# Kernel tuning notes

Hardware: AMD Instinct MI355X
Metric: run time of the kernel (lower is better)

## Reference

```python
import jax, jax.numpy as jnp
import numpy as np

B, IN, E, NCLS = 1024, 784, 256, 10
BRAIN, ADIM, NJUMPS = 4, 3, 4
N = BRAIN ** ADIM  # 64 blocks
TAU = 1.0
_GKEY = jax.random.key(42)  # fixed key -> deterministic gumbel noise


def _gumbel_softmax_hard(key, logits):
    u = jax.random.uniform(key, logits.shape, minval=1e-6, maxval=1.0 - 1e-6)
    g = -jnp.log(-jnp.log(u))
    y = jax.nn.softmax((logits + g) / TAU, axis=-1)
    hard = jax.nn.one_hot(jnp.argmax(y, axis=-1), logits.shape[-1], dtype=y.dtype)
    return jax.lax.stop_gradient(hard - y) + y  # straight-through


def _next_address(state, key, at0_W1, at0_b1, at0_W2, at0_b2):
    # always uses block 0's address_transform (as in the original forward)
    h = jax.nn.relu(state @ at0_W1 + at0_b1)
    logits = (h @ at0_W2 + at0_b2).reshape(state.shape[0], ADIM, BRAIN)
    return _gumbel_softmax_hard(key, logits)  # (B, ADIM, BRAIN) one-hot


def _all_blocks(state, st_W1, st_b1, st_W2, st_b2):
    # state: (B,E); st_W*: (N,E,E) stored (in,out). Two batched GEMMs over all N blocks.
    h = jax.nn.relu(jnp.einsum('be,neh->bnh', state, st_W1) + st_b1[None])
    h = jax.nn.relu(jnp.einsum('bnh,nhg->bng', h, st_W2) + st_b2[None])
    norm = jnp.linalg.norm(state, axis=1, keepdims=True)  # (B,1), norm of INPUT state
    return h / (norm[:, :, None] + 1e-6)  # (B,N,E)


def _flatten_onehot(oh):
    # (B, ADIM, BRAIN) -> (B, BRAIN**ADIM) via iterated outer product
    b = oh.shape[0]
    fw = oh[:, 0, :]
    for d in range(1, oh.shape[1]):
        fw = (fw[:, :, None] * oh[:, d, None, :]).reshape(b, -1)
    return fw


def _forward(x, W_emb, b_emb, st_W1, st_b1, st_W2, st_b2,
             at0_W1, at0_b1, at0_W2, at0_b2, out_W1, out_b1, out_W2, out_b2):
    bsz = x.shape[0]
    state = x.reshape(bsz, -1) @ W_emb + b_emb
    initial_state = state
    current_address = _next_address(state, jax.random.fold_in(_GKEY, 0),
                                    at0_W1, at0_b1, at0_W2, at0_b2)
    exited = jnp.zeros((bsz,), dtype=bool)
    exit_states = jnp.zeros_like(state)
    exit_addresses = jnp.zeros_like(current_address)
    for i in range(NJUMPS):  # fixed small jump count; early-break replaced by masking (same math)
        active = ~exited
        bw = _flatten_onehot(current_address)                      # (B,N)
        allout = _all_blocks(state, st_W1, st_b1, st_W2, st_b2)    # (B,N,E)
        new_state = jnp.einsum('bn,bne->be', bw, allout)
        new_address = _next_address(new_state, jax.random.fold_in(_GKEY, i + 1),
                                    at0_W1, at0_b1, at0_W2, at0_b2)
        idx = jnp.argmax(new_address, axis=2)
        is_origin = jnp.all(idx == 0, axis=1) & active
        exit_states = jnp.where(is_origin[:, None], new_state, exit_states)
        exit_addresses = jnp.where(is_origin[:, None, None], new_address, exit_addresses)
        exited = exited | is_origin
        state = jnp.where(active[:, None], new_state, state)
        current_address = jnp.where(active[:, None, None], new_address, current_address)
    final_address = jnp.where(exited[:, None, None], exit_addresses, current_address)
    bw = _flatten_onehot(final_address)
    # original code computes block_out twice and keeps the one using `state` (bug-faithful)
    allout = _all_blocks(state, st_W1, st_b1, st_W2, st_b2)
    final_output = jnp.einsum('bn,bne->be', bw, allout) + initial_state
    h = jax.nn.relu(final_output @ out_W1 + out_b1)
    return h @ out_W2 + out_b2  # (B, NCLS)


def setup_inputs() -> dict:
    key = jax.random.key(0)
    ks = jax.random.split(key, 16)
    s = 0.02
    return {
        'x': jax.random.normal(ks[0], (B, IN), jnp.float32),
        'W_emb': jax.random.normal(ks[1], (IN, E), jnp.float32) * s,
        'b_emb': jnp.zeros((E,), jnp.float32),
        'st_W1': jax.random.normal(ks[2], (N, E, E), jnp.float32) * s,
        'st_b1': jnp.zeros((N, E), jnp.float32),
        'st_W2': jax.random.normal(ks[3], (N, E, E), jnp.float32) * s,
        'st_b2': jnp.zeros((N, E), jnp.float32),
        'at0_W1': jax.random.normal(ks[4], (E, E), jnp.float32) * s,
        'at0_b1': jnp.zeros((E,), jnp.float32),
        'at0_W2': jax.random.normal(ks[5], (E, ADIM * BRAIN), jnp.float32) * s,
        'at0_b2': jnp.zeros((ADIM * BRAIN,), jnp.float32),
        'out_W1': jax.random.normal(ks[6], (E, E), jnp.float32) * s,
        'out_b1': jnp.zeros((E,), jnp.float32),
        'out_W2': jax.random.normal(ks[7], (E, NCLS), jnp.float32) * s,
        'out_b2': jnp.zeros((NCLS,), jnp.float32),
    }


def reference(x, W_emb, b_emb, st_W1, st_b1, st_W2, st_b2,
              at0_W1, at0_b1, at0_W2, at0_b2, out_W1, out_b1, out_W2, out_b2):
    return _forward(x, W_emb, b_emb, st_W1, st_b1, st_W2, st_b2,
                    at0_W1, at0_b1, at0_W2, at0_b2, out_W1, out_b1, out_W2, out_b2)
```

## Files before the change

kernel.cpp:

```cpp
#include <hip/hip_runtime.h>
#include <stdint.h>


#define BATCH 1024
#define EDIM  256
#define INDIM 784
#define GRID_BE 192

__host__ __device__ inline uint32_t rotl32(uint32_t x, uint32_t d) {
  return (x << d) | (x >> (32u - d));
}
__host__ __device__ inline void threefry2x32(uint32_t k0, uint32_t k1,
                                             uint32_t x0, uint32_t x1,
                                             uint32_t* o0, uint32_t* o1) {
  uint32_t ks2 = k0 ^ k1 ^ 0x1BD11BDAu;
  x0 += k0; x1 += k1;
#define TF_R(a) { x0 += x1; x1 = rotl32(x1, a); x1 ^= x0; }
  TF_R(13) TF_R(15) TF_R(26) TF_R(6)   x0 += k1;  x1 += ks2 + 1u;
  TF_R(17) TF_R(29) TF_R(16) TF_R(24)  x0 += ks2; x1 += k0  + 2u;
  TF_R(13) TF_R(15) TF_R(26) TF_R(6)   x0 += k0;  x1 += k1  + 3u;
  TF_R(17) TF_R(29) TF_R(16) TF_R(24)  x0 += k1;  x1 += ks2 + 4u;
  TF_R(13) TF_R(15) TF_R(26) TF_R(6)   x0 += ks2; x1 += k0  + 5u;
#undef TF_R
  *o0 = x0; *o1 = x1;
}
__device__ inline uint32_t jax_bits12288(uint32_t k0, uint32_t k1, uint32_t L) {
  uint32_t o0, o1;
  if (L < 6144u) { threefry2x32(k0, k1, L, L + 6144u, &o0, &o1); return o0; }
  else           { threefry2x32(k0, k1, L - 6144u, L, &o0, &o1); return o1; }
}
__device__ inline float jax_uniform(uint32_t bits) {
  const float minv = 1e-6f;
  const float maxv = (float)(1.0 - 1e-06);
  const float span = maxv - minv;
  uint32_t fb = (bits >> 9) | 0x3f800000u;
  float f = __uint_as_float(fb) - 1.0f;
  float u = __fadd_rn(__fmul_rn(f, span), minv);
  return fmaxf(minv, u);
}

__global__ __launch_bounds__(1024) void k_embed(
    const float* __restrict__ x, const float* __restrict__ Wemb,
    const float* __restrict__ bemb,
    float* __restrict__ stateA, float* __restrict__ initial,
    int* __restrict__ count0) {
  __shared__ float XS[8 * INDIM];
  __shared__ float P[8][128][9];
  const int t = threadIdx.x;
  if (blockIdx.x == 0 && t < 64) count0[t] = 0;
  const int rg = blockIdx.x >> 1, ch = blockIdx.x & 1;
  const int jl = t & 127, ks = t >> 7;

  {
    const float4* src = (const float4*)(x + (size_t)rg * 8 * INDIM);
    float4* dst = (float4*)XS;
    for (int p = t; p < (8 * INDIM) / 4; p += 1024) dst[p] = src[p];
  }
  __syncthreads();

  const int col = ch * 128 + jl;
  const int kb = (ks < 4) ? ks * 100 : 400 + (ks - 4) * 96;
  const int ke = kb + ((ks < 4) ? 100 : 96);
  float a[8] = {0.f,0.f,0.f,0.f,0.f,0.f,0.f,0.f};
#pragma unroll 2
  for (int k = kb; k < ke; k += 4) {
    const float w0 = Wemb[(k+0)*EDIM + col], w1 = Wemb[(k+1)*EDIM + col],
                w2 = Wemb[(k+2)*EDIM + col], w3 = Wemb[(k+3)*EDIM + col];
#pragma unroll
    for (int i = 0; i < 8; i++) {
      const float4 s4 = *(const float4*)&XS[i * INDIM + k];
      a[i] = fmaf(s4.x, w0, a[i]); a[i] = fmaf(s4.y, w1, a[i]);
      a[i] = fmaf(s4.z, w2, a[i]); a[i] = fmaf(s4.w, w3, a[i]);
    }
  }
#pragma unroll
  for (int q = 0; q < 8; q++) P[ks][jl][q] = a[q];
  __syncthreads();
  {
    const int c2 = t & 127, i = t >> 7;
    float s = 0.f;
#pragma unroll
    for (int w = 0; w < 8; w++) s += P[w][c2][i];
    s += bemb[ch * 128 + c2];
    const size_t idx = (size_t)(rg * 8 + i) * EDIM + ch * 128 + c2;
    stateA[idx] = s; initial[idx] = s;
  }
}

__global__ __launch_bounds__(1024) void k_addr(
    const float* __restrict__ state,
    const float* __restrict__ aW1, const float* __restrict__ ab1,
    const float* __restrict__ aW2, const float* __restrict__ ab2,
    int* __restrict__ exited, int* __restrict__ n_next, int* __restrict__ count,
    float* __restrict__ sout, int step, uint32_t fk0, uint32_t fk1) {
  __shared__ float XS[4 * EDIM];
  __shared__ float P[4][256][5];
  __shared__ float H[EDIM][4];
  __shared__ float P2[16][4][16];
  __shared__ float vals[4][12];
  __shared__ int   flags[4];
  const int t = threadIdx.x, b0 = blockIdx.x * 4;

  XS[t] = state[(size_t)b0 * EDIM + t];
  __syncthreads();

  const int j = t & 255, ks = t >> 8;
  const int kb = ks * 64;
  float a[4] = {0.f,0.f,0.f,0.f};
#pragma unroll 2
  for (int k = kb; k < kb + 64; k += 4) {
    const float w0 = aW1[(k+0)*EDIM + j], w1 = aW1[(k+1)*EDIM + j],
                w2 = aW1[(k+2)*EDIM + j], w3 = aW1[(k+3)*EDIM + j];
#pragma unroll
    for (int i = 0; i < 4; i++) {
      const float4 s4 = *(const float4*)&XS[i * EDIM + k];
      a[i] = fmaf(s4.x, w0, a[i]); a[i] = fmaf(s4.y, w1, a[i]);
      a[i] = fmaf(s4.z, w2, a[i]); a[i] = fmaf(s4.w, w3, a[i]);
    }
  }
#pragma unroll
  for (int q = 0; q < 4; q++) P[ks][j][q] = a[q];
  __syncthreads();
  {
    const int j2 = t & 255, i = t >> 8;
    float s = P[0][j2][i] + P[1][j2][i] + P[2][j2][i] + P[3][j2][i] + ab1[j2];
    H[j2][i] = fmaxf(s, 0.f);
  }
  __syncthreads();
  {
    const int c = t & 15, i = (t >> 4) & 3, ksl = t >> 6;
    float a2 = 0.f;
    if (c < 12) {
      const int k0 = ksl * 16;
#pragma unroll 4
      for (int k = k0; k < k0 + 16; k++)
        a2 = fmaf(H[k][i], aW2[k * 12 + c], a2);
    }
    P2[ksl][i][c] = a2;
  }
  __syncthreads();
  if (t < 48) {
    const int i = t / 12, c = t % 12;
    float s = 0.f;
#pragma unroll
    for (int w = 0; w < 16; w++) s += P2[w][i][c];
    const float logit = s + ab2[c];
    const uint32_t L = (uint32_t)((b0 + i) * 12 + c);
    const float u = jax_uniform(jax_bits12288(fk0, fk1, L));
    const float g = -logf(-logf(u));
    vals[i][c] = logit + g;
  }
  __syncthreads();
  if (t < 4) {
    const int b = b0 + t;
    int idx0 = 0, idx1 = 0, idx2 = 0;
    { float best = vals[t][0];
#pragma unroll
      for (int c = 1; c < 4; c++) { float v = vals[t][c];     if (v > best) { best = v; idx0 = c; } } }
    { float best = vals[t][4];
#pragma unroll
      for (int c = 1; c < 4; c++) { float v = vals[t][4 + c]; if (v > best) { best = v; idx1 = c; } } }
    { float best = vals[t][8];
#pragma unroll
      for (int c = 1; c < 4; c++) { float v = vals[t][8 + c]; if (v > best) { best = v; idx2 = c; } } }
    const int nn = idx0 * 16 + idx1 * 4 + idx2;
    int nxt;
    if (step == 0)      { exited[b] = 0; nxt = nn; }
    else if (step < 4)  {
      if (exited[b])      nxt = -1;
      else if (nn == 0) { exited[b] = 1; nxt = -1; }
      else                nxt = nn;
    } else                nxt = exited[b] ? 0 : nn;
    n_next[b] = nxt; flags[t] = nxt;
    if (nxt >= 0) atomicAdd(&count[nxt], 1);
  }
  __syncthreads();
  {
    const int i = t >> 8, jj = t & 255;
    if (flags[i] < 0) sout[(size_t)(b0 + i) * EDIM + jj] = XS[i * EDIM + jj];
  }
}

__global__ __launch_bounds__(1024) void k_blocks(
    const float* __restrict__ sin,
    const float* __restrict__ W1, const float* __restrict__ b1,
    const float* __restrict__ W2, const float* __restrict__ b2,
    const int* __restrict__ count, const int* __restrict__ n_next,
    const float* __restrict__ initial, float* __restrict__ sout,
    int* __restrict__ count_next, int is_final) {
  __shared__ float XS[8 * EDIM];
  __shared__ float P[4][256][9];
  __shared__ float H[EDIM][12];
  __shared__ int   meta[4];
  __shared__ int   rowsl[8];
  __shared__ float denom[8];
  __shared__ int   wcnt[16], wbase[16];
  const int t = threadIdx.x, c = blockIdx.x;
  if (c == 0 && t < 64) count_next[t] = 0;
  if (t < 8) rowsl[t] = 0;
  if (t < 64) {
    const int cnt = count[t];
    const int nch = (cnt + 7) >> 3;
    int icnt = cnt, inch = nch;
#pragma unroll
    for (int d = 1; d < 64; d <<= 1) {
      int t1 = __shfl_up(icnt, d), t2 = __shfl_up(inch, d);
      if (t >= d) { icnt += t1; inch += t2; }
    }
    const int ench = inch - nch;
    const int total = __shfl(inch, 63);
    if (t == 0) meta[3] = total;
    if (c >= ench && c < ench + nch) {
      meta[0] = t; meta[1] = c - ench;
      meta[2] = min(8, cnt - (c - ench) * 8);
    }
  }
  __syncthreads();
  if (c >= meta[3]) return;
  const int n = meta[0], local = meta[1], m = meta[2];

  {
    const bool flag = (n_next[t] == n);
    const unsigned long long bal = __ballot(flag);
    const int wid = t >> 6, lane = t & 63;
    if (lane == 0) wcnt[wid] = __popcll(bal);
    __syncthreads();
    if (t == 0) { int s = 0; for (int w = 0; w < 16; w++) { wbase[w] = s; s += wcnt[w]; } }
    __syncthreads();
    if (flag) {
      const int rank = wbase[wid] + __popcll(bal & ((1ull << lane) - 1ull));
      const int r0 = local * 8;
      if (rank >= r0 && rank < r0 + 8) rowsl[rank - r0] = t;
    }
    __syncthreads();
  }

  if (t < 512) {
    const int i = t >> 6, q = t & 63;
    const int row = rowsl[min(i, m - 1)] & 1023;
    const float4 v = *(const float4*)(sin + (size_t)row * EDIM + q * 4);
    ((float4*)XS)[t] = v;
    float sq = v.x*v.x + v.y*v.y + v.z*v.z + v.w*v.w;
#pragma unroll
    for (int d = 32; d >= 1; d >>= 1) sq += __shfl_xor(sq, d);
    if (q == 0) denom[i] = sqrtf(sq) + 1e-6f;
  }
  __syncthreads();

  const int j = t & 255, ks = t >> 8;
  const int kb = ks * 64;
  const float* W1n = W1 + (size_t)n * EDIM * EDIM;
  {
    float a[8] = {0.f,0.f,0.f,0.f,0.f,0.f,0.f,0.f};
#pragma unroll 2
    for (int k = kb; k < kb + 64; k += 4) {
      const float w0 = W1n[(k+0)*EDIM + j], w1 = W1n[(k+1)*EDIM + j],
                  w2 = W1n[(k+2)*EDIM + j], w3 = W1n[(k+3)*EDIM + j];
#pragma unroll
      for (int i = 0; i < 8; i++) {
        const float4 s4 = *(const float4*)&XS[i * EDIM + k];
        a[i] = fmaf(s4.x, w0, a[i]); a[i] = fmaf(s4.y, w1, a[i]);
        a[i] = fmaf(s4.z, w2, a[i]); a[i] = fmaf(s4.w, w3, a[i]);
      }
    }
#pragma unroll
    for (int q = 0; q < 8; q++) P[ks][j][q] = a[q];
  }
  __syncthreads();
  {
    const int j2 = t & 255, ih = t >> 8;
    const float bb = b1[(size_t)n * EDIM + j2];
#pragma unroll
    for (int qq = 0; qq < 2; qq++) {
      const int i = ih + qq * 4;
      float s = P[0][j2][i] + P[1][j2][i] + P[2][j2][i] + P[3][j2][i] + bb;
      H[j2][i] = fmaxf(s, 0.f);
    }
  }
  __syncthreads();
  const float* W2n = W2 + (size_t)n * EDIM * EDIM;
  {
    float a[8] = {0.f,0.f,0.f,0.f,0.f,0.f,0.f,0.f};
#pragma unroll 4
    for (int k = kb; k < kb + 64; k++) {
      const float w = W2n[k*EDIM + j];
      const float4 h0 = *(const float4*)&H[k][0];
      const float4 h1 = *(const float4*)&H[k][4];
      a[0] = fmaf(h0.x, w, a[0]); a[1] = fmaf(h0.y, w, a[1]);
      a[2] = fmaf(h0.z, w, a[2]); a[3] = fmaf(h0.w, w, a[3]);
      a[4] = fmaf(h1.x, w, a[4]); a[5] = fmaf(h1.y, w, a[5]);
      a[6] = fmaf(h1.z, w, a[6]); a[7] = fmaf(h1.w, w, a[7]);
    }
#pragma unroll
    for (int q = 0; q < 8; q++) P[ks][j][q] = a[q];
  }
  __syncthreads();
  {
    const int col = t & 255, ih = t >> 8;
    const float bb2 = b2[(size_t)n * EDIM + col];
#pragma unroll
    for (int qq = 0; qq < 2; qq++) {
      const int i = ih + qq * 4;
      if (i < m) {
        float s = P[0][col][i] + P[1][col][i] + P[2][col][i] + P[3][col][i] + bb2;
        float v = fmaxf(s, 0.f) / denom[i];
        const int row = rowsl[i] & 1023;
        if (is_final) v += initial[(size_t)row * EDIM + col];
        sout[(size_t)row * EDIM + col] = v;
      }
    }
  }
}

__global__ __launch_bounds__(1024) void k_head(
    const float* __restrict__ fin,
    const float* __restrict__ oW1, const float* __restrict__ ob1,
    const float* __restrict__ oW2, const float* __restrict__ ob2,
    float* __restrict__ out) {
  __shared__ float XS[4 * EDIM];
  __shared__ float P[4][256][5];
  __shared__ float H[EDIM][4];
  __shared__ float P2[16][4][16];
  const int t = threadIdx.x, b0 = blockIdx.x * 4;
  XS[t] = fin[(size_t)b0 * EDIM + t];
  __syncthreads();
  const int j = t & 255, ks = t >> 8;
  const int kb = ks * 64;
  float a[4] = {0.f,0.f,0.f,0.f};
#pragma unroll 2
  for (int k = kb; k < kb + 64; k += 4) {
    const float w0 = oW1[(k+0)*EDIM + j], w1 = oW1[(k+1)*EDIM + j],
                w2 = oW1[(k+2)*EDIM + j], w3 = oW1[(k+3)*EDIM + j];
#pragma unroll
    for (int i = 0; i < 4; i++) {
      const float4 s4 = *(const float4*)&XS[i * EDIM + k];
      a[i] = fmaf(s4.x, w0, a[i]); a[i] = fmaf(s4.y, w1, a[i]);
      a[i] = fmaf(s4.z, w2, a[i]); a[i] = fmaf(s4.w, w3, a[i]);
    }
  }
#pragma unroll
  for (int q = 0; q < 4; q++) P[ks][j][q] = a[q];
  __syncthreads();
  {
    const int j2 = t & 255, i = t >> 8;
    float s = P[0][j2][i] + P[1][j2][i] + P[2][j2][i] + P[3][j2][i] + ob1[j2];
    H[j2][i] = fmaxf(s, 0.f);
  }
  __syncthreads();
  {
    const int c = t & 15, i = (t >> 4) & 3, ksl = t >> 6;
    float a2 = 0.f;
    if (c < 10) {
      const int k0 = ksl * 16;
#pragma unroll 4
      for (int k = k0; k < k0 + 16; k++)
        a2 = fmaf(H[k][i], oW2[k * 10 + c], a2);
    }
    P2[ksl][i][c] = a2;
  }
  __syncthreads();
  if (t < 40) {
    const int i = t / 10, c = t % 10;
    float s = 0.f;
#pragma unroll
    for (int w = 0; w < 16; w++) s += P2[w][i][c];
    out[(size_t)(b0 + i) * 10 + c] = s + ob2[c];
  }
}

extern "C" void kernel_launch(void* const* d_in, const int* in_sizes, int n_in,
                              void* d_out, int out_size, void* d_ws, size_t ws_size,
                              hipStream_t stream) {
  const float* x    = (const float*)d_in[0];
  const float* Wemb = (const float*)d_in[1];
  const float* bemb = (const float*)d_in[2];
  const float* stW1 = (const float*)d_in[3];
  const float* stb1 = (const float*)d_in[4];
  const float* stW2 = (const float*)d_in[5];
  const float* stb2 = (const float*)d_in[6];
  const float* aW1  = (const float*)d_in[7];
  const float* ab1  = (const float*)d_in[8];
  const float* aW2  = (const float*)d_in[9];
  const float* ab2  = (const float*)d_in[10];
  const float* oW1  = (const float*)d_in[11];
  const float* ob1  = (const float*)d_in[12];
  const float* oW2  = (const float*)d_in[13];
  const float* ob2  = (const float*)d_in[14];
  float* out = (float*)d_out;

  char* ws = (char*)d_ws;
  auto alloc = [&](size_t bytes) { char* p = ws; ws += (bytes + 255) & ~(size_t)255; return p; };
  float* stateA  = (float*)alloc((size_t)BATCH * EDIM * 4);
  float* stateB  = (float*)alloc((size_t)BATCH * EDIM * 4);
  float* initial = (float*)alloc((size_t)BATCH * EDIM * 4);
  float* finalb  = (float*)alloc((size_t)BATCH * EDIM * 4);
  int* exited = (int*)alloc(BATCH * 4);
  int* n_next = (int*)alloc(BATCH * 4);
  int* counters[2];
  counters[0] = (int*)alloc(64 * 4);
  counters[1] = (int*)alloc(64 * 4);

  uint32_t fk0[5], fk1[5];
  for (uint32_t s = 0; s < 5; s++) threefry2x32(0u, 42u, 0u, s, &fk0[s], &fk1[s]);

  k_embed<<<256, 1024, 0, stream>>>(x, Wemb, bemb, stateA, initial, counters[0]);

  float* cur = stateA;
  float* nxt = stateB;
  for (int j = 0; j < 5; j++) {
    int* cnt  = counters[j & 1];
    int* cntN = counters[(j + 1) & 1];
    float* dst = (j < 4) ? nxt : finalb;
    k_addr<<<BATCH / 4, 1024, 0, stream>>>(cur, aW1, ab1, aW2, ab2,
        exited, n_next, cnt, dst, j, fk0[j], fk1[j]);
    k_blocks<<<GRID_BE, 1024, 0, stream>>>(cur, stW1, stb1, stW2, stb2,
        cnt, n_next, initial, dst, cntN, (j == 4) ? 1 : 0);
    if (j < 4) { float* tmp = cur; cur = nxt; nxt = tmp; }
  }
  k_head<<<BATCH / 4, 1024, 0, stream>>>(finalb, oW1, ob1, oW2, ob2, out);
}
```

Before: 265.9 us.

## Fuse address routing into block kernels and head into final block kernel

Merges the embedding and first address computation into one kernel, fuses each jump's address MLP and gumbel argmax into the block-expert kernel, and folds the output head into the final block kernel. Per-block routing counts are rebuilt locally from a per-step routing array, which drops the global atomic counters, the exited array and the ping-pong state buffers. Launches go from twelve to six and the state round-trips between them are removed. In exchange, each block recomputes a histogram over the whole batch, and the address MLP runs on padded groups of eight rows.

```diff
diff --git a/kernel.cpp b/kernel.cpp
--- a/kernel.cpp
+++ b/kernel.cpp
@@ -5,7 +5,7 @@
 #define BATCH 1024
 #define EDIM  256
 #define INDIM 784
-#define GRID_BE 192
+#define GRID_B 192
 
 __host__ __device__ inline uint32_t rotl32(uint32_t x, uint32_t d) {
   return (x << d) | (x >> (32u - d));
@@ -38,97 +38,98 @@
   float u = __fadd_rn(__fmul_rn(f, span), minv);
   return fmaxf(minv, u);
 }
-
-__global__ __launch_bounds__(1024) void k_embed(
+__device__ inline float gumbel_val(int s, int b, int c) {
+  uint32_t fk0, fk1;
+  threefry2x32(0u, 42u, 0u, (uint32_t)s, &fk0, &fk1);
+  const uint32_t L = (uint32_t)(b * 12 + c);
+  const float u = jax_uniform(jax_bits12288(fk0, fk1, L));
+  return -logf(-logf(u));
+}
+
+__device__ inline int addr_argmax(const float* v) {
+  int i0 = 0, i1 = 0, i2 = 0;
+  { float b = v[0];
+    for (int c = 1; c < 4; c++) { float x = v[c];     if (x > b) { b = x; i0 = c; } } }
+  { float b = v[4];
+    for (int c = 1; c < 4; c++) { float x = v[4 + c]; if (x > b) { b = x; i1 = c; } } }
+  { float b = v[8];
+    for (int c = 1; c < 4; c++) { float x = v[8 + c]; if (x > b) { b = x; i2 = c; } } }
+  return i0 * 16 + i1 * 4 + i2;
+}
+
+__global__ __launch_bounds__(1024, 4) void k_embed_a0(
     const float* __restrict__ x, const float* __restrict__ Wemb,
     const float* __restrict__ bemb,
-    float* __restrict__ stateA, float* __restrict__ initial,
-    int* __restrict__ count0) {
-  __shared__ float XS[8 * INDIM];
-  __shared__ float P[8][128][9];
-  const int t = threadIdx.x;
-  if (blockIdx.x == 0 && t < 64) count0[t] = 0;
-  const int rg = blockIdx.x >> 1, ch = blockIdx.x & 1;
-  const int jl = t & 127, ks = t >> 7;
-
-  {
-    const float4* src = (const float4*)(x + (size_t)rg * 8 * INDIM);
-    float4* dst = (float4*)XS;
-    for (int p = t; p < (8 * INDIM) / 4; p += 1024) dst[p] = src[p];
-  }
-  __syncthreads();
-
-  const int col = ch * 128 + jl;
-  const int kb = (ks < 4) ? ks * 100 : 400 + (ks - 4) * 96;
-  const int ke = kb + ((ks < 4) ? 100 : 96);
-  float a[8] = {0.f,0.f,0.f,0.f,0.f,0.f,0.f,0.f};
-#pragma unroll 2
-  for (int k = kb; k < ke; k += 4) {
-    const float w0 = Wemb[(k+0)*EDIM + col], w1 = Wemb[(k+1)*EDIM + col],
-                w2 = Wemb[(k+2)*EDIM + col], w3 = Wemb[(k+3)*EDIM + col];
-#pragma unroll
-    for (int i = 0; i < 8; i++) {
-      const float4 s4 = *(const float4*)&XS[i * INDIM + k];
-      a[i] = fmaf(s4.x, w0, a[i]); a[i] = fmaf(s4.y, w1, a[i]);
-      a[i] = fmaf(s4.z, w2, a[i]); a[i] = fmaf(s4.w, w3, a[i]);
-    }
-  }
-#pragma unroll
-  for (int q = 0; q < 8; q++) P[ks][jl][q] = a[q];
-  __syncthreads();
-  {
-    const int c2 = t & 127, i = t >> 7;
-    float s = 0.f;
-#pragma unroll
-    for (int w = 0; w < 8; w++) s += P[w][c2][i];
-    s += bemb[ch * 128 + c2];
-    const size_t idx = (size_t)(rg * 8 + i) * EDIM + ch * 128 + c2;
-    stateA[idx] = s; initial[idx] = s;
-  }
-}
-
-__global__ __launch_bounds__(1024) void k_addr(
-    const float* __restrict__ state,
     const float* __restrict__ aW1, const float* __restrict__ ab1,
     const float* __restrict__ aW2, const float* __restrict__ ab2,
-    int* __restrict__ exited, int* __restrict__ n_next, int* __restrict__ count,
-    float* __restrict__ sout, int step, uint32_t fk0, uint32_t fk1) {
-  __shared__ float XS[4 * EDIM];
+    float* __restrict__ state, float* __restrict__ initial,
+    int* __restrict__ nn_all) {
+  __shared__ float XS[4 * INDIM];
   __shared__ float P[4][256][5];
+  __shared__ float SS[4 * EDIM];
   __shared__ float H[EDIM][4];
   __shared__ float P2[16][4][16];
   __shared__ float vals[4][12];
-  __shared__ int   flags[4];
   const int t = threadIdx.x, b0 = blockIdx.x * 4;
 
-  XS[t] = state[(size_t)b0 * EDIM + t];
+  {
+    const float4* src = (const float4*)(x + (size_t)b0 * INDIM);
+    float4* dst = (float4*)XS;
+    for (int p = t; p < INDIM; p += 1024) dst[p] = src[p];
+  }
   __syncthreads();
 
   const int j = t & 255, ks = t >> 8;
-  const int kb = ks * 64;
-  float a[4] = {0.f,0.f,0.f,0.f};
+  {
+    const int kb = ks * 196;
+    float a[4] = {0.f,0.f,0.f,0.f};
 #pragma unroll 2
-  for (int k = kb; k < kb + 64; k += 4) {
-    const float w0 = aW1[(k+0)*EDIM + j], w1 = aW1[(k+1)*EDIM + j],
-                w2 = aW1[(k+2)*EDIM + j], w3 = aW1[(k+3)*EDIM + j];
-#pragma unroll
-    for (int i = 0; i < 4; i++) {
-      const float4 s4 = *(const float4*)&XS[i * EDIM + k];
-      a[i] = fmaf(s4.x, w0, a[i]); a[i] = fmaf(s4.y, w1, a[i]);
-      a[i] = fmaf(s4.z, w2, a[i]); a[i] = fmaf(s4.w, w3, a[i]);
-    }
-  }
-#pragma unroll
-  for (int q = 0; q < 4; q++) P[ks][j][q] = a[q];
+    for (int k = kb; k < kb + 196; k += 4) {
+      const float w0 = Wemb[(k+0)*EDIM + j], w1 = Wemb[(k+1)*EDIM + j],
+                  w2 = Wemb[(k+2)*EDIM + j], w3 = Wemb[(k+3)*EDIM + j];
+#pragma unroll
+      for (int i = 0; i < 4; i++) {
+        const float4 s4 = *(const float4*)&XS[i * INDIM + k];
+        a[i] = fmaf(s4.x, w0, a[i]); a[i] = fmaf(s4.y, w1, a[i]);
+        a[i] = fmaf(s4.z, w2, a[i]); a[i] = fmaf(s4.w, w3, a[i]);
+      }
+    }
+#pragma unroll
+    for (int q = 0; q < 4; q++) P[ks][j][q] = a[q];
+  }
   __syncthreads();
   {
     const int j2 = t & 255, i = t >> 8;
+    float s = P[0][j2][i] + P[1][j2][i] + P[2][j2][i] + P[3][j2][i] + bemb[j2];
+    SS[i * EDIM + j2] = s;
+    const size_t idx = (size_t)(b0 + i) * EDIM + j2;
+    state[idx] = s; initial[idx] = s;
+  }
+  __syncthreads();
+
+  { const int kb = ks * 64;
+    float a[4] = {0.f,0.f,0.f,0.f};
+#pragma unroll 2
+    for (int k = kb; k < kb + 64; k += 4) {
+      const float w0 = aW1[(k+0)*EDIM + j], w1 = aW1[(k+1)*EDIM + j],
+                  w2 = aW1[(k+2)*EDIM + j], w3 = aW1[(k+3)*EDIM + j];
+#pragma unroll
+      for (int i = 0; i < 4; i++) {
+        const float4 s4 = *(const float4*)&SS[i * EDIM + k];
+        a[i] = fmaf(s4.x, w0, a[i]); a[i] = fmaf(s4.y, w1, a[i]);
+        a[i] = fmaf(s4.z, w2, a[i]); a[i] = fmaf(s4.w, w3, a[i]);
+      }
+    }
+#pragma unroll
+    for (int q = 0; q < 4; q++) P[ks][j][q] = a[q];
+  }
+  __syncthreads();
+  { const int j2 = t & 255, i = t >> 8;
     float s = P[0][j2][i] + P[1][j2][i] + P[2][j2][i] + P[3][j2][i] + ab1[j2];
     H[j2][i] = fmaxf(s, 0.f);
   }
   __syncthreads();
-  {
-    const int c = t & 15, i = (t >> 4) & 3, ksl = t >> 6;
+  { const int c = t & 15, i = (t >> 4) & 3, ksl = t >> 6;
     float a2 = 0.f;
     if (c < 12) {
       const int k0 = ksl * 16;
@@ -144,62 +145,44 @@
     float s = 0.f;
 #pragma unroll
     for (int w = 0; w < 16; w++) s += P2[w][i][c];
-    const float logit = s + ab2[c];
-    const uint32_t L = (uint32_t)((b0 + i) * 12 + c);
-    const float u = jax_uniform(jax_bits12288(fk0, fk1, L));
-    const float g = -logf(-logf(u));
-    vals[i][c] = logit + g;
-  }
-  __syncthreads();
-  if (t < 4) {
-    const int b = b0 + t;
-    int idx0 = 0, idx1 = 0, idx2 = 0;
-    { float best = vals[t][0];
-#pragma unroll
-      for (int c = 1; c < 4; c++) { float v = vals[t][c];     if (v > best) { best = v; idx0 = c; } } }
-    { float best = vals[t][4];
-#pragma unroll
-      for (int c = 1; c < 4; c++) { float v = vals[t][4 + c]; if (v > best) { best = v; idx1 = c; } } }
-    { float best = vals[t][8];
-#pragma unroll
-      for (int c = 1; c < 4; c++) { float v = vals[t][8 + c]; if (v > best) { best = v; idx2 = c; } } }
-    const int nn = idx0 * 16 + idx1 * 4 + idx2;
-    int nxt;
-    if (step == 0)      { exited[b] = 0; nxt = nn; }
-    else if (step < 4)  {
-      if (exited[b])      nxt = -1;
-      else if (nn == 0) { exited[b] = 1; nxt = -1; }
-      else                nxt = nn;
-    } else                nxt = exited[b] ? 0 : nn;
-    n_next[b] = nxt; flags[t] = nxt;
-    if (nxt >= 0) atomicAdd(&count[nxt], 1);
-  }
-  __syncthreads();
-  {
-    const int i = t >> 8, jj = t & 255;
-    if (flags[i] < 0) sout[(size_t)(b0 + i) * EDIM + jj] = XS[i * EDIM + jj];
-  }
-}
-
-__global__ __launch_bounds__(1024) void k_blocks(
-    const float* __restrict__ sin,
+    vals[i][c] = s + ab2[c] + gumbel_val(0, b0 + i, c);
+  }
+  __syncthreads();
+  if (t < 4) nn_all[b0 + t] = addr_argmax(vals[t]);
+}
+
+struct BShared {
+  float XS[8 * EDIM];
+  float P[4][256][9];
+  float H[EDIM][12];
+  float P2[8][8][16];
+  float vals[8][12];
+  float denom[8];
+  int rowsl[8];
+  int hist[64];
+  int meta[4];
+  int wcnt[16], wbase[16];
+};
+
+
+__global__ __launch_bounds__(1024, 4) void k_block_mid(
+    float* __restrict__ state,
     const float* __restrict__ W1, const float* __restrict__ b1,
     const float* __restrict__ W2, const float* __restrict__ b2,
-    const int* __restrict__ count, const int* __restrict__ n_next,
-    const float* __restrict__ initial, float* __restrict__ sout,
-    int* __restrict__ count_next, int is_final) {
-  __shared__ float XS[8 * EDIM];
-  __shared__ float P[4][256][9];
-  __shared__ float H[EDIM][12];
-  __shared__ int   meta[4];
-  __shared__ int   rowsl[8];
-  __shared__ float denom[8];
-  __shared__ int   wcnt[16], wbase[16];
+    const float* __restrict__ aW1, const float* __restrict__ ab1,
+    const float* __restrict__ aW2, const float* __restrict__ ab2,
+    int* __restrict__ nn_all, int rstep) {
+  __shared__ BShared sm;
   const int t = threadIdx.x, c = blockIdx.x;
-  if (c == 0 && t < 64) count_next[t] = 0;
-  if (t < 8) rowsl[t] = 0;
+  const int* nnj = nn_all + rstep * BATCH;
+
+  if (t < 64) sm.hist[t] = 0;
+  __syncthreads();
+  const int vmy = nnj[t];
+  if (vmy >= 0) atomicAdd(&sm.hist[vmy], 1);
+  __syncthreads();
   if (t < 64) {
-    const int cnt = count[t];
+    const int cnt = sm.hist[t];
     const int nch = (cnt + 7) >> 3;
     int icnt = cnt, inch = nch;
 #pragma unroll
@@ -208,49 +191,48 @@
       if (t >= d) { icnt += t1; inch += t2; }
     }
     const int ench = inch - nch;
-    const int total = __shfl(inch, 63);
-    if (t == 0) meta[3] = total;
+    if (t == 63) sm.meta[3] = inch;
     if (c >= ench && c < ench + nch) {
-      meta[0] = t; meta[1] = c - ench;
-      meta[2] = min(8, cnt - (c - ench) * 8);
-    }
-  }
-  __syncthreads();
-  if (c >= meta[3]) return;
-  const int n = meta[0], local = meta[1], m = meta[2];
+      sm.meta[0] = t; sm.meta[1] = c - ench;
+      sm.meta[2] = min(8, cnt - (c - ench) * 8);
+    }
+  }
+  if (t < 8) sm.rowsl[t] = 0;
+  __syncthreads();
+  if (c >= sm.meta[3]) return;
+  const int n = sm.meta[0], local = sm.meta[1], m = sm.meta[2];
 
   {
-    const bool flag = (n_next[t] == n);
+    const bool flag = (vmy == n);
     const unsigned long long bal = __ballot(flag);
     const int wid = t >> 6, lane = t & 63;
-    if (lane == 0) wcnt[wid] = __popcll(bal);
+    if (lane == 0) sm.wcnt[wid] = __popcll(bal);
     __syncthreads();
-    if (t == 0) { int s = 0; for (int w = 0; w < 16; w++) { wbase[w] = s; s += wcnt[w]; } }
+    if (t == 0) { int s = 0; for (int w = 0; w < 16; w++) { sm.wbase[w] = s; s += sm.wcnt[w]; } }
     __syncthreads();
     if (flag) {
-      const int rank = wbase[wid] + __popcll(bal & ((1ull << lane) - 1ull));
+      const int rank = sm.wbase[wid] + __popcll(bal & ((1ull << lane) - 1ull));
       const int r0 = local * 8;
-      if (rank >= r0 && rank < r0 + 8) rowsl[rank - r0] = t;
+      if (rank >= r0 && rank < r0 + 8) sm.rowsl[rank - r0] = t;
     }
     __syncthreads();
   }
 
   if (t < 512) {
     const int i = t >> 6, q = t & 63;
-    const int row = rowsl[min(i, m - 1)] & 1023;
-    const float4 v = *(const float4*)(sin + (size_t)row * EDIM + q * 4);
-    ((float4*)XS)[t] = v;
+    const int row = sm.rowsl[min(i, m - 1)] & 1023;
+    const float4 v = *(const float4*)(state + (size_t)row * EDIM + q * 4);
+    ((float4*)sm.XS)[t] = v;
     float sq = v.x*v.x + v.y*v.y + v.z*v.z + v.w*v.w;
 #pragma unroll
     for (int d = 32; d >= 1; d >>= 1) sq += __shfl_xor(sq, d);
-    if (q == 0) denom[i] = sqrtf(sq) + 1e-6f;
+    if (q == 0) sm.denom[i] = sqrtf(sq) + 1e-6f;
   }
   __syncthreads();
 
   const int j = t & 255, ks = t >> 8;
   const int kb = ks * 64;
-  const float* W1n = W1 + (size_t)n * EDIM * EDIM;
-  {
+  { const float* W1n = W1 + (size_t)n * EDIM * EDIM;
     float a[8] = {0.f,0.f,0.f,0.f,0.f,0.f,0.f,0.f};
 #pragma unroll 2
     for (int k = kb; k < kb + 64; k += 4) {
@@ -258,41 +240,226 @@
                   w2 = W1n[(k+2)*EDIM + j], w3 = W1n[(k+3)*EDIM + j];
 #pragma unroll
       for (int i = 0; i < 8; i++) {
-        const float4 s4 = *(const float4*)&XS[i * EDIM + k];
+        const float4 s4 = *(const float4*)&sm.XS[i * EDIM + k];
         a[i] = fmaf(s4.x, w0, a[i]); a[i] = fmaf(s4.y, w1, a[i]);
         a[i] = fmaf(s4.z, w2, a[i]); a[i] = fmaf(s4.w, w3, a[i]);
       }
     }
 #pragma unroll
-    for (int q = 0; q < 8; q++) P[ks][j][q] = a[q];
-  }
-  __syncthreads();
-  {
-    const int j2 = t & 255, ih = t >> 8;
+    for (int q = 0; q < 8; q++) sm.P[ks][j][q] = a[q];
+  }
+  __syncthreads();
+  { const int j2 = t & 255, ih = t >> 8;
     const float bb = b1[(size_t)n * EDIM + j2];
 #pragma unroll
     for (int qq = 0; qq < 2; qq++) {
       const int i = ih + qq * 4;
-      float s = P[0][j2][i] + P[1][j2][i] + P[2][j2][i] + P[3][j2][i] + bb;
-      H[j2][i] = fmaxf(s, 0.f);
-    }
-  }
-  __syncthreads();
-  const float* W2n = W2 + (size_t)n * EDIM * EDIM;
-  {
+      float s = sm.P[0][j2][i] + sm.P[1][j2][i] + sm.P[2][j2][i] + sm.P[3][j2][i] + bb;
+      sm.H[j2][i] = fmaxf(s, 0.f);
+    }
+  }
+  __syncthreads();
+  { const float* W2n = W2 + (size_t)n * EDIM * EDIM;
     float a[8] = {0.f,0.f,0.f,0.f,0.f,0.f,0.f,0.f};
 #pragma unroll 4
     for (int k = kb; k < kb + 64; k++) {
       const float w = W2n[k*EDIM + j];
-      const float4 h0 = *(const float4*)&H[k][0];
-      const float4 h1 = *(const float4*)&H[k][4];
+      const float4 h0 = *(const float4*)&sm.H[k][0];
+      const float4 h1 = *(const float4*)&sm.H[k][4];
       a[0] = fmaf(h0.x, w, a[0]); a[1] = fmaf(h0.y, w, a[1]);
       a[2] = fmaf(h0.z, w, a[2]); a[3] = fmaf(h0.w, w, a[3]);
       a[4] = fmaf(h1.x, w, a[4]); a[5] = fmaf(h1.y, w, a[5]);
       a[6] = fmaf(h1.z, w, a[6]); a[7] = fmaf(h1.w, w, a[7]);
     }
 #pragma unroll
-    for (int q = 0; q < 8; q++) P[ks][j][q] = a[q];
+    for (int q = 0; q < 8; q++) sm.P[ks][j][q] = a[q];
+  }
+  __syncthreads();
+  { const int col = t & 255, ih = t >> 8;
+    const float bb2 = b2[(size_t)n * EDIM + col];
+#pragma unroll
+    for (int qq = 0; qq < 2; qq++) {
+      const int i = ih + qq * 4;
+      if (i < m) {
+        float s = sm.P[0][col][i] + sm.P[1][col][i] + sm.P[2][col][i] + sm.P[3][col][i] + bb2;
+        float v = fmaxf(s, 0.f) / sm.denom[i];
+        const int row = sm.rowsl[i] & 1023;
+        state[(size_t)row * EDIM + col] = v;
+        sm.XS[i * EDIM + col] = v;
+      }
+    }
+  }
+  __syncthreads();
+
+  { float a[8] = {0.f,0.f,0.f,0.f,0.f,0.f,0.f,0.f};
+#pragma unroll 2
+    for (int k = kb; k < kb + 64; k += 4) {
+      const float w0 = aW1[(k+0)*EDIM + j], w1 = aW1[(k+1)*EDIM + j],
+                  w2 = aW1[(k+2)*EDIM + j], w3 = aW1[(k+3)*EDIM + j];
+#pragma unroll
+      for (int i = 0; i < 8; i++) {
+        const float4 s4 = *(const float4*)&sm.XS[i * EDIM + k];
+        a[i] = fmaf(s4.x, w0, a[i]); a[i] = fmaf(s4.y, w1, a[i]);
+        a[i] = fmaf(s4.z, w2, a[i]); a[i] = fmaf(s4.w, w3, a[i]);
+      }
+    }
+#pragma unroll
+    for (int q = 0; q < 8; q++) sm.P[ks][j][q] = a[q];
+  }
+  __syncthreads();
+  { const int j2 = t & 255, ih = t >> 8;
+    const float bb = ab1[j2];
+#pragma unroll
+    for (int qq = 0; qq < 2; qq++) {
+      const int i = ih + qq * 4;
+      float s = sm.P[0][j2][i] + sm.P[1][j2][i] + sm.P[2][j2][i] + sm.P[3][j2][i] + bb;
+      sm.H[j2][i] = fmaxf(s, 0.f);
+    }
+  }
+  __syncthreads();
+  { const int cc = t & 15, i = (t >> 4) & 7, ksl = t >> 7;
+    float a2 = 0.f;
+    if (cc < 12) {
+      const int k0 = ksl * 32;
+#pragma unroll 4
+      for (int k = k0; k < k0 + 32; k++)
+        a2 = fmaf(sm.H[k][i], aW2[k * 12 + cc], a2);
+    }
+    sm.P2[ksl][i][cc] = a2;
+  }
+  __syncthreads();
+  if (t < 96) {
+    const int i = t / 12, cc = t % 12;
+    float s = 0.f;
+#pragma unroll
+    for (int w = 0; w < 8; w++) s += sm.P2[w][i][cc];
+    const int row = sm.rowsl[i] & 1023;
+    sm.vals[i][cc] = s + ab2[cc] + gumbel_val(rstep + 1, row, cc);
+  }
+  __syncthreads();
+  if (t < 8 && t < m) {
+    const int b = sm.rowsl[t] & 1023;
+    const int nn = addr_argmax(sm.vals[t]);
+    const int s = rstep + 1;
+    if (s < 4) {
+      if (nn == 0) {
+        for (int q = s; q <= 4; q++) nn_all[q * BATCH + b] = -1;
+      } else nn_all[s * BATCH + b] = nn;
+    } else {
+      nn_all[4 * BATCH + b] = nn;
+    }
+  }
+}
+
+__global__ __launch_bounds__(1024, 4) void k_block_final(
+    const float* __restrict__ state,
+    const float* __restrict__ W1, const float* __restrict__ b1,
+    const float* __restrict__ W2, const float* __restrict__ b2,
+    const float* __restrict__ initial,
+    const float* __restrict__ oW1, const float* __restrict__ ob1,
+    const float* __restrict__ oW2, const float* __restrict__ ob2,
+    const int* __restrict__ nn4, float* __restrict__ out) {
+  __shared__ BShared sm;
+  const int t = threadIdx.x, c = blockIdx.x;
+
+  if (t < 64) sm.hist[t] = 0;
+  __syncthreads();
+  int vmy = nn4[t];
+  if (vmy < 0) vmy = 0;
+  atomicAdd(&sm.hist[vmy], 1);
+  __syncthreads();
+  if (t < 64) {
+    const int cnt = sm.hist[t];
+    const int nch = (cnt + 7) >> 3;
+    int icnt = cnt, inch = nch;
+#pragma unroll
+    for (int d = 1; d < 64; d <<= 1) {
+      int t1 = __shfl_up(icnt, d), t2 = __shfl_up(inch, d);
+      if (t >= d) { icnt += t1; inch += t2; }
+    }
+    const int ench = inch - nch;
+    if (t == 63) sm.meta[3] = inch;
+    if (c >= ench && c < ench + nch) {
+      sm.meta[0] = t; sm.meta[1] = c - ench;
+      sm.meta[2] = min(8, cnt - (c - ench) * 8);
+    }
+  }
+  if (t < 8) sm.rowsl[t] = 0;
+  __syncthreads();
+  if (c >= sm.meta[3]) return;
+  const int n = sm.meta[0], local = sm.meta[1], m = sm.meta[2];
+
+  {
+    const bool flag = (vmy == n);
+    const unsigned long long bal = __ballot(flag);
+    const int wid = t >> 6, lane = t & 63;
+    if (lane == 0) sm.wcnt[wid] = __popcll(bal);
+    __syncthreads();
+    if (t == 0) { int s = 0; for (int w = 0; w < 16; w++) { sm.wbase[w] = s; s += sm.wcnt[w]; } }
+    __syncthreads();
+    if (flag) {
+      const int rank = sm.wbase[wid] + __popcll(bal & ((1ull << lane) - 1ull));
+      const int r0 = local * 8;
+      if (rank >= r0 && rank < r0 + 8) sm.rowsl[rank - r0] = t;
+    }
+    __syncthreads();
+  }
+
+  if (t < 512) {
+    const int i = t >> 6, q = t & 63;
+    const int row = sm.rowsl[min(i, m - 1)] & 1023;
+    const float4 v = *(const float4*)(state + (size_t)row * EDIM + q * 4);
+    ((float4*)sm.XS)[t] = v;
+    float sq = v.x*v.x + v.y*v.y + v.z*v.z + v.w*v.w;
+#pragma unroll
+    for (int d = 32; d >= 1; d >>= 1) sq += __shfl_xor(sq, d);
+    if (q == 0) sm.denom[i] = sqrtf(sq) + 1e-6f;
+  }
+  __syncthreads();
+
+  const int j = t & 255, ks = t >> 8;
+  const int kb = ks * 64;
+  { const float* W1n = W1 + (size_t)n * EDIM * EDIM;
+    float a[8] = {0.f,0.f,0.f,0.f,0.f,0.f,0.f,0.f};
+#pragma unroll 2
+    for (int k = kb; k < kb + 64; k += 4) {
+      const float w0 = W1n[(k+0)*EDIM + j], w1 = W1n[(k+1)*EDIM + j],
+                  w2 = W1n[(k+2)*EDIM + j], w3 = W1n[(k+3)*EDIM + j];
+#pragma unroll
+      for (int i = 0; i < 8; i++) {
+        const float4 s4 = *(const float4*)&sm.XS[i * EDIM + k];
+        a[i] = fmaf(s4.x, w0, a[i]); a[i] = fmaf(s4.y, w1, a[i]);
+        a[i] = fmaf(s4.z, w2, a[i]); a[i] = fmaf(s4.w, w3, a[i]);
+      }
+    }
+#pragma unroll
+    for (int q = 0; q < 8; q++) sm.P[ks][j][q] = a[q];
+  }
+  __syncthreads();
+  { const int j2 = t & 255, ih = t >> 8;
+    const float bb = b1[(size_t)n * EDIM + j2];
+#pragma unroll
+    for (int qq = 0; qq < 2; qq++) {
+      const int i = ih + qq * 4;
+      float s = sm.P[0][j2][i] + sm.P[1][j2][i] + sm.P[2][j2][i] + sm.P[3][j2][i] + bb;
+      sm.H[j2][i] = fmaxf(s, 0.f);
+    }
+  }
+  __syncthreads();
+  { const float* W2n = W2 + (size_t)n * EDIM * EDIM;
+    float a[8] = {0.f,0.f,0.f,0.f,0.f,0.f,0.f,0.f};
+#pragma unroll 4
+    for (int k = kb; k < kb + 64; k++) {
+      const float w = W2n[k*EDIM + j];
+      const float4 h0 = *(const float4*)&sm.H[k][0];
+      const float4 h1 = *(const float4*)&sm.H[k][4];
+      a[0] = fmaf(h0.x, w, a[0]); a[1] = fmaf(h0.y, w, a[1]);
+      a[2] = fmaf(h0.z, w, a[2]); a[3] = fmaf(h0.w, w, a[3]);
+      a[4] = fmaf(h1.x, w, a[4]); a[5] = fmaf(h1.y, w, a[5]);
+      a[6] = fmaf(h1.z, w, a[6]); a[7] = fmaf(h1.w, w, a[7]);
+    }
+#pragma unroll
+    for (int q = 0; q < 8; q++) sm.P[ks][j][q] = a[q];
   }
   __syncthreads();
   {
@@ -302,69 +469,62 @@
     for (int qq = 0; qq < 2; qq++) {
       const int i = ih + qq * 4;
       if (i < m) {
-        float s = P[0][col][i] + P[1][col][i] + P[2][col][i] + P[3][col][i] + bb2;
-        float v = fmaxf(s, 0.f) / denom[i];
-        const int row = rowsl[i] & 1023;
-        if (is_final) v += initial[(size_t)row * EDIM + col];
-        sout[(size_t)row * EDIM + col] = v;
-      }
-    }
-  }
-}
-
-__global__ __launch_bounds__(1024) void k_head(
-    const float* __restrict__ fin,
-    const float* __restrict__ oW1, const float* __restrict__ ob1,
-    const float* __restrict__ oW2, const float* __restrict__ ob2,
-    float* __restrict__ out) {
-  __shared__ float XS[4 * EDIM];
-  __shared__ float P[4][256][5];
-  __shared__ float H[EDIM][4];
-  __shared__ float P2[16][4][16];
-  const int t = threadIdx.x, b0 = blockIdx.x * 4;
-  XS[t] = fin[(size_t)b0 * EDIM + t];
-  __syncthreads();
-  const int j = t & 255, ks = t >> 8;
-  const int kb = ks * 64;
-  float a[4] = {0.f,0.f,0.f,0.f};
+        float s = sm.P[0][col][i] + sm.P[1][col][i] + sm.P[2][col][i] + sm.P[3][col][i] + bb2;
+        float v = fmaxf(s, 0.f) / sm.denom[i];
+        const int row = sm.rowsl[i] & 1023;
+        v += initial[(size_t)row * EDIM + col];
+        sm.XS[i * EDIM + col] = v;
+      }
+    }
+  }
+  __syncthreads();
+
+  { float a[8] = {0.f,0.f,0.f,0.f,0.f,0.f,0.f,0.f};
 #pragma unroll 2
-  for (int k = kb; k < kb + 64; k += 4) {
-    const float w0 = oW1[(k+0)*EDIM + j], w1 = oW1[(k+1)*EDIM + j],
-                w2 = oW1[(k+2)*EDIM + j], w3 = oW1[(k+3)*EDIM + j];
-#pragma unroll
-    for (int i = 0; i < 4; i++) {
-      const float4 s4 = *(const float4*)&XS[i * EDIM + k];
-      a[i] = fmaf(s4.x, w0, a[i]); a[i] = fmaf(s4.y, w1, a[i]);
-      a[i] = fmaf(s4.z, w2, a[i]); a[i] = fmaf(s4.w, w3, a[i]);
-    }
-  }
-#pragma unroll
-  for (int q = 0; q < 4; q++) P[ks][j][q] = a[q];
-  __syncthreads();
-  {
-    const int j2 = t & 255, i = t >> 8;
-    float s = P[0][j2][i] + P[1][j2][i] + P[2][j2][i] + P[3][j2][i] + ob1[j2];
-    H[j2][i] = fmaxf(s, 0.f);
-  }
-  __syncthreads();
-  {
-    const int c = t & 15, i = (t >> 4) & 3, ksl = t >> 6;
+    for (int k = kb; k < kb + 64; k += 4) {
+      const float w0 = oW1[(k+0)*EDIM + j], w1 = oW1[(k+1)*EDIM + j],
+                  w2 = oW1[(k+2)*EDIM + j], w3 = oW1[(k+3)*EDIM + j];
+#pragma unroll
+      for (int i = 0; i < 8; i++) {
+        const float4 s4 = *(const float4*)&sm.XS[i * EDIM + k];
+        a[i] = fmaf(s4.x, w0, a[i]); a[i] = fmaf(s4.y, w1, a[i]);
+        a[i] = fmaf(s4.z, w2, a[i]); a[i] = fmaf(s4.w, w3, a[i]);
+      }
+    }
+#pragma unroll
+    for (int q = 0; q < 8; q++) sm.P[ks][j][q] = a[q];
+  }
+  __syncthreads();
+  { const int j2 = t & 255, ih = t >> 8;
+    const float bb = ob1[j2];
+#pragma unroll
+    for (int qq = 0; qq < 2; qq++) {
+      const int i = ih + qq * 4;
+      float s = sm.P[0][j2][i] + sm.P[1][j2][i] + sm.P[2][j2][i] + sm.P[3][j2][i] + bb;
+      sm.H[j2][i] = fmaxf(s, 0.f);
+    }
+  }
+  __syncthreads();
+  { const int cc = t & 15, i = (t >> 4) & 7, ksl = t >> 7;
     float a2 = 0.f;
-    if (c < 10) {
-      const int k0 = ksl * 16;
+    if (cc < 10) {
+      const int k0 = ksl * 32;
 #pragma unroll 4
-      for (int k = k0; k < k0 + 16; k++)
-        a2 = fmaf(H[k][i], oW2[k * 10 + c], a2);
-    }
-    P2[ksl][i][c] = a2;
-  }
-  __syncthreads();
-  if (t < 40) {
-    const int i = t / 10, c = t % 10;
-    float s = 0.f;
-#pragma unroll
-    for (int w = 0; w < 16; w++) s += P2[w][i][c];
-    out[(size_t)(b0 + i) * 10 + c] = s + ob2[c];
+      for (int k = k0; k < k0 + 32; k++)
+        a2 = fmaf(sm.H[k][i], oW2[k * 10 + cc], a2);
+    }
+    sm.P2[ksl][i][cc] = a2;
+  }
+  __syncthreads();
+  if (t < 80) {
+    const int i = t / 10, cc = t % 10;
+    if (i < m) {
+      float s = 0.f;
+#pragma unroll
+      for (int w = 0; w < 8; w++) s += sm.P2[w][i][cc];
+      const int row = sm.rowsl[i] & 1023;
+      out[(size_t)row * 10 + cc] = s + ob2[cc];
+    }
   }
 }
 
@@ -390,32 +550,16 @@
 
   char* ws = (char*)d_ws;
   auto alloc = [&](size_t bytes) { char* p = ws; ws += (bytes + 255) & ~(size_t)255; return p; };
-  float* stateA  = (float*)alloc((size_t)BATCH * EDIM * 4);
-  float* stateB  = (float*)alloc((size_t)BATCH * EDIM * 4);
+  float* state   = (float*)alloc((size_t)BATCH * EDIM * 4);
   float* initial = (float*)alloc((size_t)BATCH * EDIM * 4);
-  float* finalb  = (float*)alloc((size_t)BATCH * EDIM * 4);
-  int* exited = (int*)alloc(BATCH * 4);
-  int* n_next = (int*)alloc(BATCH * 4);
-  int* counters[2];
-  counters[0] = (int*)alloc(64 * 4);
-  counters[1] = (int*)alloc(64 * 4);
-
-  uint32_t fk0[5], fk1[5];
-  for (uint32_t s = 0; s < 5; s++) threefry2x32(0u, 42u, 0u, s, &fk0[s], &fk1[s]);
-
-  k_embed<<<256, 1024, 0, stream>>>(x, Wemb, bemb, stateA, initial, counters[0]);
-
-  float* cur = stateA;
-  float* nxt = stateB;
-  for (int j = 0; j < 5; j++) {
-    int* cnt  = counters[j & 1];
-    int* cntN = counters[(j + 1) & 1];
-    float* dst = (j < 4) ? nxt : finalb;
-    k_addr<<<BATCH / 4, 1024, 0, stream>>>(cur, aW1, ab1, aW2, ab2,
-        exited, n_next, cnt, dst, j, fk0[j], fk1[j]);
-    k_blocks<<<GRID_BE, 1024, 0, stream>>>(cur, stW1, stb1, stW2, stb2,
-        cnt, n_next, initial, dst, cntN, (j == 4) ? 1 : 0);
-    if (j < 4) { float* tmp = cur; cur = nxt; nxt = tmp; }
-  }
-  k_head<<<BATCH / 4, 1024, 0, stream>>>(finalb, oW1, ob1, oW2, ob2, out);
-}
+  int*   nn_all  = (int*)alloc(5 * BATCH * 4);
+
+  k_embed_a0<<<BATCH / 4, 1024, 0, stream>>>(x, Wemb, bemb, aW1, ab1, aW2, ab2,
+                                             state, initial, nn_all);
+  for (int j = 0; j < 4; j++)
+    k_block_mid<<<GRID_B, 1024, 0, stream>>>(state, stW1, stb1, stW2, stb2,
+                                             aW1, ab1, aW2, ab2, nn_all, j);
+  k_block_final<<<GRID_B, 1024, 0, stream>>>(state, stW1, stb1, stW2, stb2,
+                                             initial, oW1, ob1, oW2, ob2,
+                                             nn_all + 4 * BATCH, out);
+}
```

After: 292.6 us. +10.0%, slower.
